# Performance work log

Hardware: AMD Instinct MI355X
Metric: run time of the kernel (lower is better)

## Reference

```python
import jax, jax.numpy as jnp
import numpy as np

CLASSES = 256
SUPERCLASSES = 16
CLASS_FACTOR = CLASSES // SUPERCLASSES
HEIGHT = 448
WIDTH = 160
BATCH = 1
CH_IN = 128
CH_R0 = 256
CH_R1 = 8


def _leaky(v):
    return jnp.where(v >= 0, v, 0.01 * v)


def _grouped1x1(x, W, b):
    # x: (B, H, Cin, W_sp); W: (H, Cout, Cin); b: (H, Cout)
    return jnp.einsum('bhcw,hoc->bhow', x, W) + b[None, :, :, None]


def setup_inputs() -> dict:
    key = jax.random.key(0)
    ks = jax.random.split(key, 16)
    s = 0.05
    return {
        'x_in': jax.random.normal(ks[0], (BATCH, CH_IN, HEIGHT, WIDTH), jnp.float32),
        'W_cl1': jax.random.normal(ks[1], (HEIGHT, 128, CH_IN), jnp.float32) * s,
        'b_cl1': jax.random.normal(ks[2], (HEIGHT, 128), jnp.float32) * s,
        'W_cl2': jax.random.normal(ks[3], (HEIGHT, 128, 128), jnp.float32) * s,
        'b_cl2': jax.random.normal(ks[4], (HEIGHT, 128), jnp.float32) * s,
        'W_cl3': jax.random.normal(ks[5], (HEIGHT, 128, 128), jnp.float32) * s,
        'b_cl3': jax.random.normal(ks[6], (HEIGHT, 128), jnp.float32) * s,
        'W_cl4': jax.random.normal(ks[7], (HEIGHT, CLASSES + 1, 128), jnp.float32) * s,
        'b_cl4': jax.random.normal(ks[8], (HEIGHT, CLASSES + 1), jnp.float32) * s,
        'W_reg1': jax.random.normal(ks[9], (HEIGHT, CH_R0, CH_IN), jnp.float32) * s,
        'b_reg1': jax.random.normal(ks[10], (HEIGHT, CH_R0), jnp.float32) * s,
        'W_cm2': jax.random.normal(ks[11], (SUPERCLASSES * HEIGHT, CH_R0, CH_R1), jnp.float32) * s,
        'b_cm2': jax.random.normal(ks[12], (SUPERCLASSES * HEIGHT, CH_R1), jnp.float32) * s,
        'W_cm3': jax.random.normal(ks[13], (CLASSES * HEIGHT, CH_R1, 1), jnp.float32) * s,
        'b_cm3': jax.random.normal(ks[14], (CLASSES * HEIGHT, 1), jnp.float32) * s,
    }


def reference(x_in, W_cl1, b_cl1, W_cl2, b_cl2, W_cl3, b_cl3, W_cl4, b_cl4,
              W_reg1, b_reg1, W_cm2, b_cm2, W_cm3, b_cm3):
    B, C, H, Wd = x_in.shape
    x = x_in.transpose(0, 2, 1, 3)  # (B, H, C, W) == grouped-conv layout
    x_r = _leaky(_grouped1x1(x, W_reg1, b_reg1))  # (B, H, CH_R0, W)
    # classification branch
    h = _leaky(_grouped1x1(x, W_cl1, b_cl1))
    h = _leaky(_grouped1x1(h, W_cl2, b_cl2))
    h = _leaky(_grouped1x1(h, W_cl3, b_cl3))
    h = _grouped1x1(h, W_cl4, b_cl4)  # (B, H, CLASSES+1, W)
    logits = h.transpose(0, 2, 1, 3)  # (B, CLASSES+1, H, W)
    cls = logits[:, :CLASSES]
    mask = _leaky(logits[:, -1:])  # (B, 1, H, W)
    inds = jnp.argmax(cls, axis=1)[:, None]  # (B, 1, H, W)
    offs = jnp.arange(H)[None, None, :, None]
    # NOTE: original flattens indices in (b, h, w) order...
    inds_r = (inds + offs * CLASSES).reshape(-1).astype(jnp.int32)
    inds_sc = (inds // CLASS_FACTOR + offs * SUPERCLASSES).reshape(-1).astype(jnp.int32)
    # ...while CondMul input rows come in (b, w, h) order (faithful to torch code).
    xr_rows = x_r.transpose(0, 3, 1, 2).reshape(-1, CH_R0)  # (B*W*H, CH_R0)
    y = _leaky(jnp.einsum('nc,nco->no', xr_rows, W_cm2[inds_sc]) + b_cm2[inds_sc])
    r = jnp.einsum('nc,nco->no', y, W_cm3[inds_r]) + b_cm3[inds_r]  # (N, 1)
    r = r.reshape(B, Wd, H, 1).transpose(0, 3, 2, 1)  # (B, 1, H, W)
    x_real = (inds.astype(jnp.float32) + r) * (1.0 / CLASSES)
    return x_real, mask
```

## Files before the change

kernel.cpp:

```cpp
#include <hip/hip_runtime.h>
#include <hip/hip_bf16.h>

#define HH 448
#define WW 160
#define NPIX (HH*WW)

typedef unsigned long long u64;
typedef _Float16 h8 __attribute__((ext_vector_type(8)));
typedef _Float16 h4 __attribute__((ext_vector_type(4)));
typedef float f32x4 __attribute__((ext_vector_type(4)));

#define MFMA16(A,B,C) __builtin_amdgcn_mfma_f32_16x16x32_f16(A,B,C,0,0,0)
#define LO_SCALE 4096.0f
#define LO_INV   (1.0f/4096.0f)

__device__ __forceinline__ float leaky(float v) { return v >= 0.f ? v : 0.01f * v; }

__device__ __forceinline__ u64 packKey(float m, int r) {
    unsigned u = __float_as_uint(m);
    u = (u & 0x80000000u) ? ~u : (u | 0x80000000u);
    return ((u64)u << 32) | (unsigned)(255 - r);
}

__device__ __forceinline__ _Float16 splitHi(float v) { return (_Float16)v; }
__device__ __forceinline__ _Float16 splitLo(float v, _Float16 hi) {
    return (_Float16)((v - (float)hi) * LO_SCALE);
}

__device__ __forceinline__ void cvtA(const float4& v0, const float4& v1, h8& ah, h8& al) {
    const float v[8] = {v0.x,v0.y,v0.z,v0.w,v1.x,v1.y,v1.z,v1.w};
#pragma unroll
    for (int j = 0; j < 8; ++j) {
        const _Float16 hi = splitHi(v[j]);
        ah[j] = hi;
        al[j] = splitLo(v[j], hi);
    }
}

__device__ __forceinline__ void gemmPass(const _Float16* lah, const _Float16* lal,
                                         const float* __restrict__ Wp,
                                         int lrow, int lg, int col0,
                                         f32x4 aH[2][5], f32x4 aL[2][5])
{
    const f32x4 zero = {0.f, 0.f, 0.f, 0.f};
#pragma unroll
    for (int i = 0; i < 2; ++i)
#pragma unroll
        for (int c = 0; c < 5; ++c) { aH[i][c] = zero; aL[i][c] = zero; }

    const float* wb0 = Wp + lrow * 128 + lg * 8;
    const float* wb1 = Wp + (16 + lrow) * 128 + lg * 8;
    float4 n00 = *(const float4*)(wb0);
    float4 n01 = *(const float4*)(wb0 + 4);
    float4 n10 = *(const float4*)(wb1);
    float4 n11 = *(const float4*)(wb1 + 4);

#pragma unroll 1
    for (int s = 0; s < 4; ++s) {
        const float4 c00 = n00, c01 = n01, c10 = n10, c11 = n11;
        if (s < 3) {
            n00 = *(const float4*)(wb0 + (s + 1) * 32);
            n01 = *(const float4*)(wb0 + (s + 1) * 32 + 4);
            n10 = *(const float4*)(wb1 + (s + 1) * 32);
            n11 = *(const float4*)(wb1 + (s + 1) * 32 + 4);
        }
        h8 Ah[2], Al[2];
        cvtA(c00, c01, Ah[0], Al[0]);
        cvtA(c10, c11, Ah[1], Al[1]);

        h8 Bh[5], Bl[5];
        const int gg = (s << 2) + lg;
#pragma unroll
        for (int c = 0; c < 5; ++c) {
            const int u = gg * 160 + col0 + (c << 4) + lrow;
            Bh[c] = *(const h8*)(lah + (u << 3));
            Bl[c] = *(const h8*)(lal + (u << 3));
        }
#pragma unroll
        for (int i = 0; i < 2; ++i)
#pragma unroll
            for (int c = 0; c < 5; ++c) {
                aH[i][c] = MFMA16(Ah[i], Bh[c], aH[i][c]);
                aL[i][c] = MFMA16(Ah[i], Bl[c], aL[i][c]);
                aL[i][c] = MFMA16(Al[i], Bh[c], aL[i][c]);
            }
    }
}

__global__ __launch_bounds__(512, 2) void kA(
    const float* __restrict__ x_in,
    const float* __restrict__ Wcl1, const float* __restrict__ bcl1,
    const float* __restrict__ Wcl2, const float* __restrict__ bcl2,
    const float* __restrict__ Wcl3, const float* __restrict__ bcl3,
    const float* __restrict__ Wcl4, const float* __restrict__ bcl4,
    const float* __restrict__ Wreg1, const float* __restrict__ breg1,
    __hip_bfloat16* __restrict__ xr, int* __restrict__ ind, float* __restrict__ out)
{
    __shared__ alignas(16) _Float16 lah[16 * 160 * 8];
    __shared__ alignas(16) _Float16 lal[16 * 160 * 8];
    u64* argb = reinterpret_cast<u64*>(lah);

    const int h = blockIdx.x;
    const int t = threadIdx.x;
    const int wvid = t >> 6;
    const int l = t & 63;
    const int lrow = l & 15, lg = l >> 4;
    const int rtp = wvid >> 1;
    const int ch = wvid & 1;
    const int col0 = ch * 80;
    const int trb = rtp * 32;

#pragma unroll 1
    for (int k = 0; k < 5; ++k) {
        const int id = t + (k << 9);
        const int g = id / 160, col = id - g * 160;
        float v[8];
#pragma unroll
        for (int j = 0; j < 8; ++j)
            v[j] = x_in[(size_t)(g * 8 + j) * 71680 + h * 160 + col];
        h8 hh, ll;
#pragma unroll
        for (int j = 0; j < 8; ++j) {
            const _Float16 hi = splitHi(v[j]);
            hh[j] = hi;
            ll[j] = splitLo(v[j], hi);
        }
        const int u = g * 160 + col;
        *(h8*)(lah + (u << 3)) = hh;
        *(h8*)(lal + (u << 3)) = ll;
    }
    __syncthreads();

    {
        const float* W1 = Wreg1 + (size_t)h * 32768;
        const float* b1 = breg1 + h * 256;
#pragma unroll 1
        for (int p = 0; p < 2; ++p) {
            const int rowOff = (p << 7) + trb;
            f32x4 aH[2][5], aL[2][5];
            gemmPass(lah, lal, W1 + rowOff * 128, lrow, lg, col0, aH, aL);
#pragma unroll
            for (int i = 0; i < 2; ++i) {
                const int r0 = rowOff + (i << 4) + (lg << 2);
                const float4 bb = *(const float4*)&b1[r0];
#pragma unroll
                for (int c = 0; c < 5; ++c) {
                    const int col = col0 + (c << 4) + lrow;
                    alignas(8) unsigned short us[4];
#pragma unroll
                    for (int r = 0; r < 4; ++r) {
                        const float a = aH[i][c][r] + aL[i][c][r] * LO_INV + ((const float*)&bb)[r];
                        __hip_bfloat16 bv = __float2bfloat16(leaky(a));
                        us[r] = *(const unsigned short*)&bv;
                    }
                    *(uint2*)(xr + (((size_t)(h * 160 + col)) << 8) + r0) = *(const uint2*)us;
                }
            }
        }
    }

#pragma unroll 1
    for (int L = 0; L < 3; ++L) {
        const float* W = (L == 0) ? Wcl1 + (size_t)h * 16384
                       : (L == 1) ? Wcl2 + (size_t)h * 16384
                                  : Wcl3 + (size_t)h * 16384;
        const float* b = (L == 0) ? bcl1 + (h << 7)
                       : (L == 1) ? bcl2 + (h << 7)
                                  : bcl3 + (h << 7);
        f32x4 aH[2][5], aL[2][5];
        gemmPass(lah, lal, W + trb * 128, lrow, lg, col0, aH, aL);
        float nv[2][5][4];
#pragma unroll
        for (int i = 0; i < 2; ++i) {
            const int r0 = trb + (i << 4) + (lg << 2);
            const float4 bb = *(const float4*)&b[r0];
#pragma unroll
            for (int c = 0; c < 5; ++c)
#pragma unroll
                for (int r = 0; r < 4; ++r)
                    nv[i][c][r] = leaky(aH[i][c][r] + aL[i][c][r] * LO_INV + ((const float*)&bb)[r]);
        }
        __syncthreads();
#pragma unroll
        for (int i = 0; i < 2; ++i) {
            const int r0 = trb + (i << 4) + (lg << 2);
            const int g = r0 >> 3, off = r0 & 7;
#pragma unroll
            for (int c = 0; c < 5; ++c) {
                const int col = col0 + (c << 4) + lrow;
                h4 wh, wl;
#pragma unroll
                for (int r = 0; r < 4; ++r) {
                    const _Float16 hi = splitHi(nv[i][c][r]);
                    wh[r] = hi;
                    wl[r] = splitLo(nv[i][c][r], hi);
                }
                *(h4*)(lah + ((g * 160 + col) << 3) + off) = wh;
                *(h4*)(lal + ((g * 160 + col) << 3) + off) = wl;
            }
        }
        __syncthreads();
    }

    if (t < 160) {
        const float* Wm = Wcl4 + (size_t)h * 32896 + 32768;
        float accm = 0.f;
#pragma unroll 2
        for (int g = 0; g < 16; ++g) {
            const h8 hv = *(const h8*)(lah + ((g * 160 + t) << 3));
            const h8 lv = *(const h8*)(lal + ((g * 160 + t) << 3));
            const float4 w0 = *(const float4*)&Wm[g * 8];
            const float4 w1 = *(const float4*)&Wm[g * 8 + 4];
            const float wv[8] = {w0.x,w0.y,w0.z,w0.w,w1.x,w1.y,w1.z,w1.w};
#pragma unroll
            for (int j = 0; j < 8; ++j)
                accm = fmaf(wv[j], (float)hv[j] + (float)lv[j] * LO_INV, accm);
        }
        out[NPIX + h * 160 + t] = leaky(accm + bcl4[h * 257 + 256]);
    }

    float mv[5]; int mr[5];
    {
        const float* W4 = Wcl4 + (size_t)h * 32896;
        const float* b4 = bcl4 + h * 257;
#pragma unroll
        for (int c = 0; c < 5; ++c) { mv[c] = -3.4e38f; mr[c] = 0; }
#pragma unroll 1
        for (int p = 0; p < 2; ++p) {
            const int rowOff = (p << 7) + trb;
            f32x4 aH[2][5], aL[2][5];
            gemmPass(lah, lal, W4 + rowOff * 128, lrow, lg, col0, aH, aL);
#pragma unroll
            for (int i = 0; i < 2; ++i) {
                const int r0 = rowOff + (i << 4) + (lg << 2);
                const float4 bb = *(const float4*)&b4[r0];
#pragma unroll
                for (int c = 0; c < 5; ++c)
#pragma unroll
                    for (int r = 0; r < 4; ++r) {
                        const float a = aH[i][c][r] + aL[i][c][r] * LO_INV + ((const float*)&bb)[r];
                        if (a > mv[c]) { mv[c] = a; mr[c] = r0 + r; }
                    }
            }
        }
    }
    __syncthreads();
    if (t < 160) argb[t] = 0ull;
    __syncthreads();
#pragma unroll
    for (int c = 0; c < 5; ++c)
        atomicMax(&argb[col0 + (c << 4) + lrow], packKey(mv[c], mr[c]));
    __syncthreads();

    if (t < 160) {
        const u64 kk = argb[t];
        ind[h * 160 + t] = 255 - (int)(kk & 0xFFu);
    }
}

__global__ __launch_bounds__(256) void kB(
    const __hip_bfloat16* __restrict__ xr, const int* __restrict__ ind,
    const float* __restrict__ Wcm2, const float* __restrict__ bcm2,
    const float* __restrict__ Wcm3, const float* __restrict__ bcm3,
    float* __restrict__ out)
{
    const int gwave = (int)((blockIdx.x * blockDim.x + threadIdx.x) >> 6);
    const int lane = threadIdx.x & 63;
    const int nwave = (int)(gridDim.x * (blockDim.x >> 6));

    for (int n = gwave; n < NPIX; n += nwave) {
        const int h_o = n % HH, w_o = n / HH;
        const int h_i = n / WW, w_i = n % WW;
        const int ig = ind[h_i * WW + w_i];
        const int sc = (ig >> 4) + (h_i << 4);
        const int rr = ig + (h_i << 8);

        const __hip_bfloat16* xp = xr + (size_t)(h_o * WW + w_o) * 256;
        const float* Wp = Wcm2 + (size_t)sc * 2048;

        float acc[8];
#pragma unroll
        for (int o = 0; o < 8; ++o) acc[o] = 0.f;

        const int c0 = lane * 4;
        const ushort4 xv4 = *(const ushort4*)((const unsigned short*)xp + c0);
        float xf[4];
        xf[0] = __uint_as_float((unsigned int)xv4.x << 16);
        xf[1] = __uint_as_float((unsigned int)xv4.y << 16);
        xf[2] = __uint_as_float((unsigned int)xv4.z << 16);
        xf[3] = __uint_as_float((unsigned int)xv4.w << 16);

#pragma unroll
        for (int i = 0; i < 4; ++i) {
            const float4* wrow = (const float4*)&Wp[(c0 + i) * 8];
            const float4 wa = wrow[0];
            const float4 wb_ = wrow[1];
            const float x = xf[i];
            acc[0] += x * wa.x;  acc[1] += x * wa.y;  acc[2] += x * wa.z;  acc[3] += x * wa.w;
            acc[4] += x * wb_.x; acc[5] += x * wb_.y; acc[6] += x * wb_.z; acc[7] += x * wb_.w;
        }
#pragma unroll
        for (int o = 0; o < 8; ++o) {
            float v = acc[o];
#pragma unroll
            for (int d = 32; d > 0; d >>= 1) v += __shfl_xor(v, d, 64);
            acc[o] = v;
        }
        float r = bcm3[rr];
        const float* b2 = bcm2 + (size_t)sc * 8;
        const float* w3 = Wcm3 + (size_t)rr * 8;
#pragma unroll
        for (int o = 0; o < 8; ++o) {
            const float y = leaky(acc[o] + b2[o]);
            r += y * w3[o];
        }
        if (lane == 0) {
            const float iv = (float)ind[h_o * WW + w_o];
            out[h_o * WW + w_o] = (iv + r) * (1.0f / 256.0f);
        }
    }
}

extern "C" void kernel_launch(void* const* d_in, const int* in_sizes, int n_in,
                              void* d_out, int out_size, void* d_ws, size_t ws_size,
                              hipStream_t stream)
{
    const float* x_in  = (const float*)d_in[0];
    const float* Wcl1  = (const float*)d_in[1];
    const float* bcl1  = (const float*)d_in[2];
    const float* Wcl2  = (const float*)d_in[3];
    const float* bcl2  = (const float*)d_in[4];
    const float* Wcl3  = (const float*)d_in[5];
    const float* bcl3  = (const float*)d_in[6];
    const float* Wcl4  = (const float*)d_in[7];
    const float* bcl4  = (const float*)d_in[8];
    const float* Wreg1 = (const float*)d_in[9];
    const float* breg1 = (const float*)d_in[10];
    const float* Wcm2  = (const float*)d_in[11];
    const float* bcm2  = (const float*)d_in[12];
    const float* Wcm3  = (const float*)d_in[13];
    const float* bcm3  = (const float*)d_in[14];

    float* out = (float*)d_out;

    __hip_bfloat16* xr = (__hip_bfloat16*)d_ws;
    int* ind = (int*)((char*)d_ws + (size_t)NPIX * 256 * sizeof(__hip_bfloat16));

    kA<<<dim3(HH), dim3(512), 0, stream>>>(x_in, Wcl1, bcl1, Wcl2, bcl2, Wcl3, bcl3,
                                           Wcl4, bcl4, Wreg1, breg1, xr, ind, out);
    kB<<<dim3(1792), dim3(256), 0, stream>>>(xr, ind, Wcm2, bcm2, Wcm3, bcm3, out);
}
```

Before: 185.2 us.

## Double kA block to 1024 threads, each wave computing one 16-row tile

kA now launches 1024 threads per block. Each wave computes a single 16-row output tile instead of two, so the per-wave MFMA work and accumulator registers are halved and more waves are available to hide latency. Launch bounds change to (1024,4) and the input staging loop is resized to match. In exchange, B fragments from LDS are loaded once per 16 rows instead of once per 32, which doubles LDS read traffic per MFMA. The tighter register budget may also cause spills.

```diff
diff --git a/kernel.cpp b/kernel.cpp
--- a/kernel.cpp
+++ b/kernel.cpp
@@ -40,54 +40,42 @@
 __device__ __forceinline__ void gemmPass(const _Float16* lah, const _Float16* lal,
                                          const float* __restrict__ Wp,
                                          int lrow, int lg, int col0,
-                                         f32x4 aH[2][5], f32x4 aL[2][5])
+                                         f32x4 aH[5], f32x4 aL[5])
 {
     const f32x4 zero = {0.f, 0.f, 0.f, 0.f};
 #pragma unroll
-    for (int i = 0; i < 2; ++i)
-#pragma unroll
-        for (int c = 0; c < 5; ++c) { aH[i][c] = zero; aL[i][c] = zero; }
+    for (int c = 0; c < 5; ++c) { aH[c] = zero; aL[c] = zero; }
 
     const float* wb0 = Wp + lrow * 128 + lg * 8;
-    const float* wb1 = Wp + (16 + lrow) * 128 + lg * 8;
     float4 n00 = *(const float4*)(wb0);
     float4 n01 = *(const float4*)(wb0 + 4);
-    float4 n10 = *(const float4*)(wb1);
-    float4 n11 = *(const float4*)(wb1 + 4);
+
+    const int ub = col0 + lrow;
 
 #pragma unroll 1
     for (int s = 0; s < 4; ++s) {
-        const float4 c00 = n00, c01 = n01, c10 = n10, c11 = n11;
+        const float4 c00 = n00, c01 = n01;
         if (s < 3) {
             n00 = *(const float4*)(wb0 + (s + 1) * 32);
             n01 = *(const float4*)(wb0 + (s + 1) * 32 + 4);
-            n10 = *(const float4*)(wb1 + (s + 1) * 32);
-            n11 = *(const float4*)(wb1 + (s + 1) * 32 + 4);
-        }
-        h8 Ah[2], Al[2];
-        cvtA(c00, c01, Ah[0], Al[0]);
-        cvtA(c10, c11, Ah[1], Al[1]);
-
-        h8 Bh[5], Bl[5];
+        }
+        h8 Ah, Al;
+        cvtA(c00, c01, Ah, Al);
+
         const int gg = (s << 2) + lg;
 #pragma unroll
         for (int c = 0; c < 5; ++c) {
-            const int u = gg * 160 + col0 + (c << 4) + lrow;
-            Bh[c] = *(const h8*)(lah + (u << 3));
-            Bl[c] = *(const h8*)(lal + (u << 3));
-        }
-#pragma unroll
-        for (int i = 0; i < 2; ++i)
-#pragma unroll
-            for (int c = 0; c < 5; ++c) {
-                aH[i][c] = MFMA16(Ah[i], Bh[c], aH[i][c]);
-                aL[i][c] = MFMA16(Ah[i], Bl[c], aL[i][c]);
-                aL[i][c] = MFMA16(Al[i], Bh[c], aL[i][c]);
-            }
-    }
-}
-
-__global__ __launch_bounds__(512, 2) void kA(
+            const int u = gg * 160 + ub + (c << 4);
+            const h8 Bh = *(const h8*)(lah + (u << 3));
+            const h8 Bl = *(const h8*)(lal + (u << 3));
+            aH[c] = MFMA16(Ah, Bh, aH[c]);
+            aL[c] = MFMA16(Ah, Bl, aL[c]);
+            aL[c] = MFMA16(Al, Bh, aL[c]);
+        }
+    }
+}
+
+__global__ __launch_bounds__(1024, 4) void kA(
     const float* __restrict__ x_in,
     const float* __restrict__ Wcl1, const float* __restrict__ bcl1,
     const float* __restrict__ Wcl2, const float* __restrict__ bcl2,
@@ -105,29 +93,31 @@
     const int wvid = t >> 6;
     const int l = t & 63;
     const int lrow = l & 15, lg = l >> 4;
-    const int rtp = wvid >> 1;
+    const int rt = wvid >> 1;
     const int ch = wvid & 1;
     const int col0 = ch * 80;
-    const int trb = rtp * 32;
-
-#pragma unroll 1
-    for (int k = 0; k < 5; ++k) {
-        const int id = t + (k << 9);
-        const int g = id / 160, col = id - g * 160;
-        float v[8];
-#pragma unroll
-        for (int j = 0; j < 8; ++j)
-            v[j] = x_in[(size_t)(g * 8 + j) * 71680 + h * 160 + col];
-        h8 hh, ll;
-#pragma unroll
-        for (int j = 0; j < 8; ++j) {
-            const _Float16 hi = splitHi(v[j]);
-            hh[j] = hi;
-            ll[j] = splitLo(v[j], hi);
-        }
-        const int u = g * 160 + col;
-        *(h8*)(lah + (u << 3)) = hh;
-        *(h8*)(lal + (u << 3)) = ll;
+    const int trb = rt * 16;
+
+#pragma unroll 1
+    for (int k = 0; k < 3; ++k) {
+        const int id = t + (k << 10);
+        if (id < 2560) {
+            const int g = id / 160, col = id - g * 160;
+            float v[8];
+#pragma unroll
+            for (int j = 0; j < 8; ++j)
+                v[j] = x_in[(size_t)(g * 8 + j) * 71680 + h * 160 + col];
+            h8 hh, ll;
+#pragma unroll
+            for (int j = 0; j < 8; ++j) {
+                const _Float16 hi = splitHi(v[j]);
+                hh[j] = hi;
+                ll[j] = splitLo(v[j], hi);
+            }
+            const int u = g * 160 + col;
+            *(h8*)(lah + (u << 3)) = hh;
+            *(h8*)(lal + (u << 3)) = ll;
+        }
     }
     __syncthreads();
 
@@ -137,24 +127,21 @@
 #pragma unroll 1
         for (int p = 0; p < 2; ++p) {
             const int rowOff = (p << 7) + trb;
-            f32x4 aH[2][5], aL[2][5];
+            f32x4 aH[5], aL[5];
             gemmPass(lah, lal, W1 + rowOff * 128, lrow, lg, col0, aH, aL);
-#pragma unroll
-            for (int i = 0; i < 2; ++i) {
-                const int r0 = rowOff + (i << 4) + (lg << 2);
-                const float4 bb = *(const float4*)&b1[r0];
-#pragma unroll
-                for (int c = 0; c < 5; ++c) {
-                    const int col = col0 + (c << 4) + lrow;
-                    alignas(8) unsigned short us[4];
-#pragma unroll
-                    for (int r = 0; r < 4; ++r) {
-                        const float a = aH[i][c][r] + aL[i][c][r] * LO_INV + ((const float*)&bb)[r];
-                        __hip_bfloat16 bv = __float2bfloat16(leaky(a));
-                        us[r] = *(const unsigned short*)&bv;
-                    }
-                    *(uint2*)(xr + (((size_t)(h * 160 + col)) << 8) + r0) = *(const uint2*)us;
+            const int r0 = rowOff + (lg << 2);
+            const float4 bb = *(const float4*)&b1[r0];
+#pragma unroll
+            for (int c = 0; c < 5; ++c) {
+                const int col = col0 + (c << 4) + lrow;
+                alignas(8) unsigned short us[4];
+#pragma unroll
+                for (int r = 0; r < 4; ++r) {
+                    const float a = aH[c][r] + aL[c][r] * LO_INV + ((const float*)&bb)[r];
+                    __hip_bfloat16 bv = __float2bfloat16(leaky(a));
+                    us[r] = *(const unsigned short*)&bv;
                 }
+                *(uint2*)(xr + (((size_t)(h * 160 + col)) << 8) + r0) = *(const uint2*)us;
             }
         }
     }
@@ -167,23 +154,18 @@
         const float* b = (L == 0) ? bcl1 + (h << 7)
                        : (L == 1) ? bcl2 + (h << 7)
                                   : bcl3 + (h << 7);
-        f32x4 aH[2][5], aL[2][5];
+        f32x4 aH[5], aL[5];
         gemmPass(lah, lal, W + trb * 128, lrow, lg, col0, aH, aL);
-        float nv[2][5][4];
-#pragma unroll
-        for (int i = 0; i < 2; ++i) {
-            const int r0 = trb + (i << 4) + (lg << 2);
-            const float4 bb = *(const float4*)&b[r0];
-#pragma unroll
-            for (int c = 0; c < 5; ++c)
-#pragma unroll
-                for (int r = 0; r < 4; ++r)
-                    nv[i][c][r] = leaky(aH[i][c][r] + aL[i][c][r] * LO_INV + ((const float*)&bb)[r]);
-        }
+        const int r0 = trb + (lg << 2);
+        const float4 bb = *(const float4*)&b[r0];
+        float nv[5][4];
+#pragma unroll
+        for (int c = 0; c < 5; ++c)
+#pragma unroll
+            for (int r = 0; r < 4; ++r)
+                nv[c][r] = leaky(aH[c][r] + aL[c][r] * LO_INV + ((const float*)&bb)[r]);
         __syncthreads();
-#pragma unroll
-        for (int i = 0; i < 2; ++i) {
-            const int r0 = trb + (i << 4) + (lg << 2);
+        {
             const int g = r0 >> 3, off = r0 & 7;
 #pragma unroll
             for (int c = 0; c < 5; ++c) {
@@ -191,9 +173,9 @@
                 h4 wh, wl;
 #pragma unroll
                 for (int r = 0; r < 4; ++r) {
-                    const _Float16 hi = splitHi(nv[i][c][r]);
+                    const _Float16 hi = splitHi(nv[c][r]);
                     wh[r] = hi;
-                    wl[r] = splitLo(nv[i][c][r], hi);
+                    wl[r] = splitLo(nv[c][r], hi);
                 }
                 *(h4*)(lah + ((g * 160 + col) << 3) + off) = wh;
                 *(h4*)(lal + ((g * 160 + col) << 3) + off) = wl;
@@ -228,20 +210,17 @@
 #pragma unroll 1
         for (int p = 0; p < 2; ++p) {
             const int rowOff = (p << 7) + trb;
-            f32x4 aH[2][5], aL[2][5];
+            f32x4 aH[5], aL[5];
             gemmPass(lah, lal, W4 + rowOff * 128, lrow, lg, col0, aH, aL);
-#pragma unroll
-            for (int i = 0; i < 2; ++i) {
-                const int r0 = rowOff + (i << 4) + (lg << 2);
-                const float4 bb = *(const float4*)&b4[r0];
-#pragma unroll
-                for (int c = 0; c < 5; ++c)
-#pragma unroll
-                    for (int r = 0; r < 4; ++r) {
-                        const float a = aH[i][c][r] + aL[i][c][r] * LO_INV + ((const float*)&bb)[r];
-                        if (a > mv[c]) { mv[c] = a; mr[c] = r0 + r; }
-                    }
-            }
+            const int r0 = rowOff + (lg << 2);
+            const float4 bb = *(const float4*)&b4[r0];
+#pragma unroll
+            for (int c = 0; c < 5; ++c)
+#pragma unroll
+                for (int r = 0; r < 4; ++r) {
+                    const float a = aH[c][r] + aL[c][r] * LO_INV + ((const float*)&bb)[r];
+                    if (a > mv[c]) { mv[c] = a; mr[c] = r0 + r; }
+                }
         }
     }
     __syncthreads();
@@ -346,7 +325,7 @@
     __hip_bfloat16* xr = (__hip_bfloat16*)d_ws;
     int* ind = (int*)((char*)d_ws + (size_t)NPIX * 256 * sizeof(__hip_bfloat16));
 
-    kA<<<dim3(HH), dim3(512), 0, stream>>>(x_in, Wcl1, bcl1, Wcl2, bcl2, Wcl3, bcl3,
-                                           Wcl4, bcl4, Wreg1, breg1, xr, ind, out);
+    kA<<<dim3(HH), dim3(1024), 0, stream>>>(x_in, Wcl1, bcl1, Wcl2, bcl2, Wcl3, bcl3,
+                                            Wcl4, bcl4, Wreg1, breg1, xr, ind, out);
     kB<<<dim3(1792), dim3(256), 0, stream>>>(xr, ind, Wcm2, bcm2, Wcm3, bcm3, out);
 }
```

Measured after the change: 180.5 us. 2.5% less time.
